# Performance work log

Measured on AMD Instinct MI355X. Metric: run time of the kernel, lower is better.

Reference implementation:

```python
import jax, jax.numpy as jnp
import numpy as np
import math

D_MODEL = 1024
EMB = 1024

def setup_inputs() -> dict:
    key = jax.random.key(0)
    ks = jax.random.split(key, 9)
    s = 1.0 / math.sqrt(EMB)
    x = jax.random.normal(ks[0], (4, 2048, EMB), dtype=jnp.float32)
    W1 = jax.random.uniform(ks[1], (EMB, EMB), minval=-s, maxval=s)
    b1 = jax.random.uniform(ks[2], (EMB,), minval=-s, maxval=s)
    W2 = jax.random.uniform(ks[3], (EMB, EMB), minval=-s, maxval=s)
    b2 = jax.random.uniform(ks[4], (EMB,), minval=-s, maxval=s)
    W3 = jax.random.uniform(ks[5], (EMB, EMB), minval=-s, maxval=s)
    b3 = jax.random.uniform(ks[6], (EMB,), minval=-s, maxval=s)
    W4 = jax.random.uniform(ks[7], (EMB, EMB), minval=-s, maxval=s)
    b4 = jax.random.uniform(ks[8], (EMB,), minval=-s, maxval=s)
    return {"x": x, "W1": W1, "b1": b1, "W2": W2, "b2": b2,
            "W3": W3, "b3": b3, "W4": W4, "b4": b4}

def reference(x, W1, b1, W2, b2, W3, b3, W4, b4):
    # Q, K, V projections (torch Linear: x @ W.T + b; here W stored as [in, out])
    Q = x @ W1 + b1          # [B, S, E]
    K = x @ W2 + b2
    V = x @ W3 + b3
    scale = 1.0 / math.sqrt(D_MODEL)
    scores = jnp.einsum('bse,bte->bst', Q, K) * scale   # [B, S, S]
    attn = jax.nn.softmax(scores, axis=-1)
    out = jnp.einsum('bst,bte->bse', attn, V)           # [B, S, E]
    return out @ W4 + b4
```

## Files before the change

kernel.cpp:

```cpp
#include <hip/hip_runtime.h>
#include <hip/hip_bf16.h>

typedef __attribute__((ext_vector_type(4))) float f32x4;
typedef __attribute__((ext_vector_type(8))) short bf16x8;

__device__ __forceinline__ void gload_lds16(const void* g, void* l) {
  __builtin_amdgcn_global_load_lds(
      (const __attribute__((address_space(1))) void*)g,
      (__attribute__((address_space(3))) void*)l, 16, 0, 0);
}

__device__ __forceinline__ unsigned short f2bf(float f) {
  union { float f; unsigned u; } x; x.f = f;
  unsigned r = x.u + 0x7fffu + ((x.u >> 16) & 1u);
  return (unsigned short)(r >> 16);
}

__device__ __forceinline__ float bf2f(unsigned short s) {
  union { unsigned u; float f; } x; x.u = (unsigned)s << 16;
  return x.f;
}

template<int N> __device__ __forceinline__ void vm_wait();
template<> __device__ __forceinline__ void vm_wait<0>() { asm volatile("s_waitcnt vmcnt(0)" ::: "memory"); }
template<> __device__ __forceinline__ void vm_wait<4>() { asm volatile("s_waitcnt vmcnt(4)" ::: "memory"); }
template<> __device__ __forceinline__ void vm_wait<6>() { asm volatile("s_waitcnt vmcnt(6)" ::: "memory"); }

#define BARRIER() asm volatile("s_barrier" ::: "memory")
#define SCHED0()  __builtin_amdgcn_sched_barrier(0)

template<int BN, int EPI, bool OUT_F32>
__global__ __launch_bounds__(512, 2)
void gemm256(const unsigned short* __restrict__ A,
             const unsigned short* __restrict__ Bt,
             const float* __restrict__ bias,
             float* __restrict__ rs,
             void* __restrict__ Cout,
             int K, int lda, int ldb, int ldc, float alpha,
             long sA, long sB, long sC)
{
  constexpr int THREADS = 512;
  constexpr int WN = BN / 64;
  constexpr int WM = 8 / WN;
  constexpr int WTM = 256 / WM;
  constexpr int M_REP = WTM / 16;
  constexpr int MH = M_REP / 2;
  constexpr int ABUFE = 256 * 64;
  constexpr int BBUFE = BN * 64;
  constexpr int BBASE = 2 * ABUFE;
  constexpr int LOADS_A = 2;
  constexpr int LOADS_B = BN / 128;
  constexpr int VM_STEADY = 2 * LOADS_B + LOADS_A;

  __shared__ __attribute__((aligned(16))) unsigned short lds[BBASE + 2 * BBUFE];

  const int gx = gridDim.x, gy = gridDim.y;
  const int lid = blockIdx.x + gx * (blockIdx.y + gy * blockIdx.z);
  const int nwg = gx * gy * gridDim.z;
  const int q = nwg >> 3, r = nwg & 7;
  const int xcd = lid & 7, idx = lid >> 3;
  const int nl = (xcd < r ? xcd * (q + 1) : r * (q + 1) + (xcd - r) * q) + idx;
  const int bx = nl % gx, by = (nl / gx) % gy, bz = nl / (gx * gy);

  const int tid = threadIdx.x, wave = tid >> 6, lane = tid & 63;
  const int wr = wave / WN, wc = wave % WN;
  const int fr = lane & 15, fq = lane >> 4, sw = fr & 7;

  A  += (size_t)bz * sA;
  Bt += (size_t)bz * sB;
  const int m0 = by * 256;
  const int n0 = bx * BN;
  const int NT = K >> 6;

  f32x4 acc[M_REP][4] = {};
  bf16x8 a[MH][2], b[4][2];

  auto stageA = [&](int t, int half) {
#pragma unroll
    for (int c = 0; c < LOADS_A; ++c) {
      const int s = c * THREADS + tid;
      const int rr = s >> 3;
      const int col = ((tid & 7) ^ (rr & 7)) * 8;
      gload_lds16(A + (size_t)(m0 + half * 128 + rr) * lda + t * 64 + col,
                  &lds[(t & 1) * ABUFE + half * (128 * 64) + s * 8]);
    }
  };
  auto stageB = [&](int t, int half) {
#pragma unroll
    for (int c = 0; c < LOADS_B; ++c) {
      const int s = c * THREADS + tid;
      const int rr = s >> 3;
      const int col = ((tid & 7) ^ (rr & 7)) * 8;
      gload_lds16(Bt + (size_t)(n0 + half * (BN / 2) + rr) * ldb + t * 64 + col,
                  &lds[BBASE + (t & 1) * BBUFE + half * ((BN / 2) * 64) + s * 8]);
    }
  };
  auto readA = [&](int buf, int mq) {
    const unsigned short* p = &lds[buf * ABUFE];
#pragma unroll
    for (int mm = 0; mm < MH; ++mm)
#pragma unroll
      for (int kk = 0; kk < 2; ++kk)
        a[mm][kk] = *(const bf16x8*)(p + (wr * WTM + mq * (WTM / 2) + mm * 16 + fr) * 64
                                       + ((kk * 4 + fq) ^ sw) * 8);
  };
  auto readB = [&](int buf, int nh) {
    const unsigned short* p = &lds[BBASE + buf * BBUFE];
#pragma unroll
    for (int nn = 0; nn < 2; ++nn)
#pragma unroll
      for (int kk = 0; kk < 2; ++kk)
        b[nh * 2 + nn][kk] = *(const bf16x8*)(p + (wc * 64 + (nh * 2 + nn) * 16 + fr) * 64
                                                + ((kk * 4 + fq) ^ sw) * 8);
  };
  auto mfmaQ = [&](int mq, int nh) {
    __builtin_amdgcn_s_setprio(1);
#pragma unroll
    for (int kk = 0; kk < 2; ++kk)
#pragma unroll
      for (int mm = 0; mm < MH; ++mm)
#pragma unroll
        for (int nn = 0; nn < 2; ++nn)
          acc[mq * MH + mm][nh * 2 + nn] = __builtin_amdgcn_mfma_f32_16x16x32_bf16(
              a[mm][kk], b[nh * 2 + nn][kk], acc[mq * MH + mm][nh * 2 + nn], 0, 0, 0);
    __builtin_amdgcn_s_setprio(0);
  };

  stageA(0, 0); stageA(0, 1); stageB(0, 0); stageB(0, 1);
  if (NT > 1) { stageB(1, 0); stageB(1, 1); stageA(1, 0); vm_wait<VM_STEADY>(); }
  else        { vm_wait<0>(); }
  BARRIER();

  for (int t = 0; t < NT; ++t) {
    const int buf = t & 1;
    readA(buf, 0); readB(buf, 0);
    BARRIER(); SCHED0();
    mfmaQ(0, 0);
    SCHED0();
    BARRIER();
    readB(buf, 1);
    if (t + 1 < NT) stageA(t + 1, 1);
    BARRIER(); SCHED0();
    mfmaQ(0, 1);
    SCHED0();
    BARRIER();
    readA(buf, 1);
    if (t + 2 < NT) stageB(t + 2, 0);
    BARRIER(); SCHED0();
    mfmaQ(1, 0);
    SCHED0();
    BARRIER();
    if (t + 2 < NT) { stageB(t + 2, 1); stageA(t + 2, 0); vm_wait<VM_STEADY>(); }
    else            { vm_wait<0>(); }
    BARRIER(); SCHED0();
    mfmaQ(1, 1);
    SCHED0();
    BARRIER();
  }

  float bvc[4];
  if (EPI == 5) {
#pragma unroll
    for (int nn = 0; nn < 4; ++nn) bvc[nn] = bias[n0 + wc * 64 + nn * 16 + fr];
  }
  if (EPI == 3) {
#pragma unroll
    for (int nn = 0; nn < 4; ++nn)
      bvc[nn] = bias[(size_t)bz * 2048 + n0 + wc * 64 + nn * 16 + fr];
  }
#pragma unroll
  for (int mm = 0; mm < M_REP; ++mm) {
    const int rbase = m0 + wr * WTM + mm * 16 + fq * 4;
#pragma unroll
    for (int j = 0; j < 4; ++j) {
      const int row = rbase + j;
      float rsc = 1.f;
      if (EPI == 5) rsc = __builtin_amdgcn_rcpf(rs[(size_t)bz * 2048 + row]);
      float part = 0.f;
#pragma unroll
      for (int nn = 0; nn < 4; ++nn) {
        const int col = n0 + wc * 64 + nn * 16 + fr;
        float v = acc[mm][nn][j];
        if      (EPI == 3) { v = __expf((v + bvc[nn]) * alpha); part += v; }
        else if (EPI == 5) v = v * rsc + bvc[nn];
        else               v = v * alpha;
        const size_t off = (size_t)bz * sC + (size_t)row * ldc + col;
        if (OUT_F32) ((float*)Cout)[off] = v;
        else         ((unsigned short*)Cout)[off] = f2bf(v);
      }
      if (EPI == 3) {
        part += __shfl_xor(part, 1); part += __shfl_xor(part, 2);
        part += __shfl_xor(part, 4); part += __shfl_xor(part, 8);
        if (fr == 0) atomicAdd(rs + (size_t)bz * 2048 + row, part);
      }
    }
  }
}

__global__ __launch_bounds__(256, 2)
void prep_gemm(const unsigned short* __restrict__ W2b, const unsigned short* __restrict__ W1b,
               const unsigned short* __restrict__ W4t, const unsigned short* __restrict__ W3b,
               unsigned short* __restrict__ Mtb, unsigned short* __restrict__ W34tb)
{
  __shared__ __attribute__((aligned(16))) unsigned short As[128 * 32];
  __shared__ __attribute__((aligned(16))) unsigned short Bs[128 * 32];
  const int which = blockIdx.z;
  const unsigned short* A  = which ? W4t : W2b;
  const unsigned short* Bt = which ? W3b : W1b;
  unsigned short* C = which ? W34tb : Mtb;

  const int tid = threadIdx.x, wave = tid >> 6, lane = tid & 63;
  const int m0 = blockIdx.y * 128, n0 = blockIdx.x * 128;
  f32x4 acc[4][4] = {};
  const int wr = wave >> 1, wc = wave & 1;
  const int fr = lane & 15, fq = lane >> 4;
  const int si0 = wave * 2, sr = lane >> 2, sce = (lane & 3) * 8;

  for (int k0 = 0; k0 < 1024; k0 += 32) {
#pragma unroll
    for (int c = 0; c < 2; ++c) {
      const int i = si0 + c, rr = i * 16 + sr;
      gload_lds16(A  + (size_t)(m0 + rr) * 1024 + k0 + sce, As + i * 512 + lane * 8);
      gload_lds16(Bt + (size_t)(n0 + rr) * 1024 + k0 + sce, Bs + i * 512 + lane * 8);
    }
    __syncthreads();
    bf16x8 af[4], bg[4];
#pragma unroll
    for (int m = 0; m < 4; ++m)
      af[m] = *(const bf16x8*)(As + (wr * 64 + m * 16 + fr) * 32 + fq * 8);
#pragma unroll
    for (int n = 0; n < 4; ++n)
      bg[n] = *(const bf16x8*)(Bs + (wc * 64 + n * 16 + fr) * 32 + fq * 8);
#pragma unroll
    for (int m = 0; m < 4; ++m)
#pragma unroll
      for (int n = 0; n < 4; ++n)
        acc[m][n] = __builtin_amdgcn_mfma_f32_16x16x32_bf16(af[m], bg[n], acc[m][n], 0, 0, 0);
    __syncthreads();
  }
#pragma unroll
  for (int m = 0; m < 4; ++m) {
    const int rbase = m0 + wr * 64 + m * 16 + fq * 4;
#pragma unroll
    for (int j = 0; j < 4; ++j)
#pragma unroll
      for (int n = 0; n < 4; ++n) {
        const int col = n0 + wc * 64 + n * 16 + fr;
        C[(size_t)(rbase + j) * 1024 + col] = f2bf(acc[m][n][j]);
      }
  }
}

__global__ __launch_bounds__(256)
void convert_kernel(const float* __restrict__ x, unsigned short* __restrict__ xb)
{
  const int idx = (blockIdx.x * 256 + threadIdx.x) * 8;
  const float4 a = *(const float4*)(x + idx);
  const float4 b = *(const float4*)(x + idx + 4);
  unsigned u0 = (unsigned)f2bf(a.x) | ((unsigned)f2bf(a.y) << 16);
  unsigned u1 = (unsigned)f2bf(a.z) | ((unsigned)f2bf(a.w) << 16);
  unsigned u2 = (unsigned)f2bf(b.x) | ((unsigned)f2bf(b.y) << 16);
  unsigned u3 = (unsigned)f2bf(b.z) | ((unsigned)f2bf(b.w) << 16);
  uint4 o; o.x = u0; o.y = u1; o.z = u2; o.w = u3;
  *(uint4*)(xb + idx) = o;
}

__global__ __launch_bounds__(256)
void convert3_kernel(const float* __restrict__ a, const float* __restrict__ b,
                     const float* __restrict__ c,
                     unsigned short* __restrict__ oa, unsigned short* __restrict__ ob,
                     unsigned short* __restrict__ oc)
{
  const float* src = (blockIdx.y == 0) ? a : (blockIdx.y == 1) ? b : c;
  unsigned short* dst = (blockIdx.y == 0) ? oa : (blockIdx.y == 1) ? ob : oc;
  const int idx = (blockIdx.x * 256 + threadIdx.x) * 8;
  const float4 p = *(const float4*)(src + idx);
  const float4 q = *(const float4*)(src + idx + 4);
  unsigned u0 = (unsigned)f2bf(p.x) | ((unsigned)f2bf(p.y) << 16);
  unsigned u1 = (unsigned)f2bf(p.z) | ((unsigned)f2bf(p.w) << 16);
  unsigned u2 = (unsigned)f2bf(q.x) | ((unsigned)f2bf(q.y) << 16);
  unsigned u3 = (unsigned)f2bf(q.z) | ((unsigned)f2bf(q.w) << 16);
  uint4 o; o.x = u0; o.y = u1; o.z = u2; o.w = u3;
  *(uint4*)(dst + idx) = o;
}

__global__ __launch_bounds__(256)
void transpose_w4_kernel(const float* __restrict__ W, unsigned short* __restrict__ out)
{
  __shared__ float t[64][65];
  const int k0 = blockIdx.y * 64;
  const int n0 = blockIdx.x * 64;
  const int tx = threadIdx.x & 63, ty = threadIdx.x >> 6;
#pragma unroll
  for (int r = ty; r < 64; r += 4)
    t[r][tx] = W[(size_t)(k0 + r) * 1024 + n0 + tx];
  __syncthreads();
#pragma unroll
  for (int r = ty; r < 64; r += 4)
    out[(size_t)(n0 + r) * 1024 + k0 + tx] = f2bf(t[tx][r]);
}

__global__ __launch_bounds__(256)
void prep_vec_kernel(const float* __restrict__ W2, const float* __restrict__ b1,
                     const unsigned short* __restrict__ W4t,
                     const float* __restrict__ b3, const float* __restrict__ b4,
                     float* __restrict__ w21, float* __restrict__ bfv)
{
  const int e = blockIdx.x * 4 + (threadIdx.x >> 6);
  const int lane = threadIdx.x & 63;
  float acc = 0.f;
  if (blockIdx.y == 0) {
#pragma unroll 4
    for (int i = 0; i < 16; ++i) {
      const int n = i * 64 + lane;
      acc += W2[(size_t)e * 1024 + n] * b1[n];
    }
#pragma unroll
    for (int o = 32; o; o >>= 1) acc += __shfl_xor(acc, o);
    if (lane == 0) w21[e] = acc;
  } else {
#pragma unroll 4
    for (int i = 0; i < 16; ++i) {
      const int j = i * 64 + lane;
      acc += bf2f(W4t[(size_t)e * 1024 + j]) * b3[j];
    }
#pragma unroll
    for (int o = 32; o; o >>= 1) acc += __shfl_xor(acc, o);
    if (lane == 0) bfv[e] = acc + b4[e];
  }
}

__global__ __launch_bounds__(256)
void v_kernel(const unsigned short* __restrict__ xb, const float* __restrict__ w21,
              float* __restrict__ v)
{
  const int i = blockIdx.x * 4 + (threadIdx.x >> 6);
  const int lane = threadIdx.x & 63;
  float acc = 0.f;
  const unsigned short* row = xb + (size_t)i * 1024;
#pragma unroll 2
  for (int it = 0; it < 2; ++it) {
    const int k0 = (it * 64 + lane) * 8;
    bf16x8 pk = *(const bf16x8*)(row + k0);
#pragma unroll
    for (int j = 0; j < 8; ++j)
      acc += bf2f(((const unsigned short*)&pk)[j]) * w21[k0 + j];
  }
#pragma unroll
  for (int o = 32; o; o >>= 1) acc += __shfl_xor(acc, o);
  if (lane == 0) v[i] = acc;
}

extern "C" void kernel_launch(void* const* d_in, const int* in_sizes, int n_in,
                              void* d_out, int out_size, void* d_ws, size_t ws_size,
                              hipStream_t stream)
{
  const float* x  = (const float*)d_in[0];
  const float* W1 = (const float*)d_in[1];
  const float* b1 = (const float*)d_in[2];
  const float* W2 = (const float*)d_in[3];
  const float* W3 = (const float*)d_in[5];
  const float* b3 = (const float*)d_in[6];
  const float* W4 = (const float*)d_in[7];
  const float* b4 = (const float*)d_in[8];

  char* ws = (char*)d_ws;
  const size_t MB = 1024 * 1024;
  unsigned short* xb    = (unsigned short*)(ws);
  unsigned short* W4t   = (unsigned short*)(ws + 16 * MB);
  unsigned short* W2b   = (unsigned short*)(ws + 18 * MB);
  unsigned short* W1b   = (unsigned short*)(ws + 20 * MB);
  unsigned short* W3b   = (unsigned short*)(ws + 22 * MB);
  unsigned short* G     = (unsigned short*)(ws + 24 * MB);
  unsigned short* Mtb   = (unsigned short*)(ws + 40 * MB);
  unsigned short* W34tb = (unsigned short*)(ws + 42 * MB);
  float*          rsum  = (float*)(ws + 44 * MB);
  float*          bfv   = (float*)(ws + 45 * MB);
  float*          w21   = (float*)(ws + 45 * MB + 8192);
  float*          vvec  = (float*)(ws + 45 * MB + 16384);
  unsigned short* Vt    = (unsigned short*)(ws + 56 * MB);
  unsigned short* S     = (unsigned short*)(ws + 72 * MB);

  convert_kernel<<<4096, 256, 0, stream>>>(x, xb);
  convert3_kernel<<<dim3(512, 3), 256, 0, stream>>>(W1, W2, W3, W1b, W2b, W3b);
  transpose_w4_kernel<<<dim3(16, 16), 256, 0, stream>>>(W4, W4t);

  prep_gemm<<<dim3(8, 8, 2), 256, 0, stream>>>(W2b, W1b, W4t, W3b, Mtb, W34tb);

  prep_vec_kernel<<<dim3(256, 2), 256, 0, stream>>>(W2, b1, W4t, b3, b4, w21, bfv);

  gemm256<128, 0, false><<<dim3(8, 32, 1), 512, 0, stream>>>(
      xb, Mtb, nullptr, nullptr, G, 1024, 1024, 1024, 1024, 1.f, 0, 0, 0);

  gemm256<128, 0, false><<<dim3(16, 4, 4), 512, 0, stream>>>(
      W34tb, xb, nullptr, nullptr, Vt, 1024, 1024, 1024, 2048, 1.f,
      0, 2048L * 1024, 1024L * 2048);

  v_kernel<<<2048, 256, 0, stream>>>(xb, w21, vvec);

  hipMemsetAsync(rsum, 0, 4 * 2048 * sizeof(float), stream);

  gemm256<256, 3, false><<<dim3(8, 8, 4), 512, 0, stream>>>(
      G, xb, vvec, rsum, S, 1024, 1024, 1024, 2048, 0.03125f,
      2048L * 1024, 2048L * 1024, 2048L * 2048);

  gemm256<128, 5, true><<<dim3(8, 8, 4), 512, 0, stream>>>(
      S, Vt, bfv, rsum, d_out, 2048, 2048, 2048, 1024, 1.f,
      2048L * 2048, 1024L * 2048, 2048L * 1024);
}
```

Before: 184.8 us.

## Merge small prep kernels and fuse the two projection GEMMs into one launch

Several small launches are combined into fewer kernels with blockIdx-based dispatch. The weight convert, W4 transpose and bias-vector kernels become one weights_prep kernel. The Mt/W34t prep GEMM, the v-vector kernel and the rsum memset become prep2, and the G and Vt projection GEMMs run as one 512-block dual launch. This cuts launch overhead and idle tails between dependent small kernels and lets the two projection GEMMs share the GPU at the same time. The bfv vector is now computed from fp32 W4 rather than the bf16 transposed copy, which changes rounding slightly. Heterogeneous blocks in one grid can cause load imbalance.

```diff
diff --git a/kernel.cpp b/kernel.cpp
--- a/kernel.cpp
+++ b/kernel.cpp
@@ -30,14 +30,15 @@
 #define SCHED0()  __builtin_amdgcn_sched_barrier(0)
 
 template<int BN, int EPI, bool OUT_F32>
-__global__ __launch_bounds__(512, 2)
-void gemm256(const unsigned short* __restrict__ A,
-             const unsigned short* __restrict__ Bt,
-             const float* __restrict__ bias,
-             float* __restrict__ rs,
-             void* __restrict__ Cout,
-             int K, int lda, int ldb, int ldc, float alpha,
-             long sA, long sB, long sC)
+__device__ __forceinline__ void gemm_body(
+    const unsigned short* __restrict__ A,
+    const unsigned short* __restrict__ Bt,
+    const float* __restrict__ bias,
+    float* __restrict__ rs,
+    void* __restrict__ Cout,
+    int K, int lda, int ldb, int ldc, float alpha,
+    long sA, long sB, long sC,
+    int bx, int by, int bz, unsigned short* lds)
 {
   constexpr int THREADS = 512;
   constexpr int WN = BN / 64;
@@ -51,16 +52,6 @@
   constexpr int LOADS_A = 2;
   constexpr int LOADS_B = BN / 128;
   constexpr int VM_STEADY = 2 * LOADS_B + LOADS_A;
-
-  __shared__ __attribute__((aligned(16))) unsigned short lds[BBASE + 2 * BBUFE];
-
-  const int gx = gridDim.x, gy = gridDim.y;
-  const int lid = blockIdx.x + gx * (blockIdx.y + gy * blockIdx.z);
-  const int nwg = gx * gy * gridDim.z;
-  const int q = nwg >> 3, r = nwg & 7;
-  const int xcd = lid & 7, idx = lid >> 3;
-  const int nl = (xcd < r ? xcd * (q + 1) : r * (q + 1) + (xcd - r) * q) + idx;
-  const int bx = nl % gx, by = (nl / gx) % gy, bz = nl / (gx * gy);
 
   const int tid = threadIdx.x, wave = tid >> 6, lane = tid & 63;
   const int wr = wave / WN, wc = wave % WN;
@@ -197,57 +188,50 @@
   }
 }
 
-__global__ __launch_bounds__(256, 2)
-void prep_gemm(const unsigned short* __restrict__ W2b, const unsigned short* __restrict__ W1b,
-               const unsigned short* __restrict__ W4t, const unsigned short* __restrict__ W3b,
-               unsigned short* __restrict__ Mtb, unsigned short* __restrict__ W34tb)
-{
-  __shared__ __attribute__((aligned(16))) unsigned short As[128 * 32];
-  __shared__ __attribute__((aligned(16))) unsigned short Bs[128 * 32];
-  const int which = blockIdx.z;
-  const unsigned short* A  = which ? W4t : W2b;
-  const unsigned short* Bt = which ? W3b : W1b;
-  unsigned short* C = which ? W34tb : Mtb;
-
-  const int tid = threadIdx.x, wave = tid >> 6, lane = tid & 63;
-  const int m0 = blockIdx.y * 128, n0 = blockIdx.x * 128;
-  f32x4 acc[4][4] = {};
-  const int wr = wave >> 1, wc = wave & 1;
-  const int fr = lane & 15, fq = lane >> 4;
-  const int si0 = wave * 2, sr = lane >> 2, sce = (lane & 3) * 8;
-
-  for (int k0 = 0; k0 < 1024; k0 += 32) {
-#pragma unroll
-    for (int c = 0; c < 2; ++c) {
-      const int i = si0 + c, rr = i * 16 + sr;
-      gload_lds16(A  + (size_t)(m0 + rr) * 1024 + k0 + sce, As + i * 512 + lane * 8);
-      gload_lds16(Bt + (size_t)(n0 + rr) * 1024 + k0 + sce, Bs + i * 512 + lane * 8);
-    }
-    __syncthreads();
-    bf16x8 af[4], bg[4];
-#pragma unroll
-    for (int m = 0; m < 4; ++m)
-      af[m] = *(const bf16x8*)(As + (wr * 64 + m * 16 + fr) * 32 + fq * 8);
-#pragma unroll
-    for (int n = 0; n < 4; ++n)
-      bg[n] = *(const bf16x8*)(Bs + (wc * 64 + n * 16 + fr) * 32 + fq * 8);
-#pragma unroll
-    for (int m = 0; m < 4; ++m)
-#pragma unroll
-      for (int n = 0; n < 4; ++n)
-        acc[m][n] = __builtin_amdgcn_mfma_f32_16x16x32_bf16(af[m], bg[n], acc[m][n], 0, 0, 0);
-    __syncthreads();
-  }
-#pragma unroll
-  for (int m = 0; m < 4; ++m) {
-    const int rbase = m0 + wr * 64 + m * 16 + fq * 4;
-#pragma unroll
-    for (int j = 0; j < 4; ++j)
-#pragma unroll
-      for (int n = 0; n < 4; ++n) {
-        const int col = n0 + wc * 64 + n * 16 + fr;
-        C[(size_t)(rbase + j) * 1024 + col] = f2bf(acc[m][n][j]);
-      }
+__device__ __forceinline__ int xcd_swz(int lid, int nwg) {
+  const int q = nwg >> 3, r = nwg & 7;
+  const int xcd = lid & 7, idx = lid >> 3;
+  return (xcd < r ? xcd * (q + 1) : r * (q + 1) + (xcd - r) * q) + idx;
+}
+
+template<int BN, int EPI, bool OUT_F32>
+__global__ __launch_bounds__(512, 2)
+void gemm256(const unsigned short* __restrict__ A,
+             const unsigned short* __restrict__ Bt,
+             const float* __restrict__ bias,
+             float* __restrict__ rs,
+             void* __restrict__ Cout,
+             int K, int lda, int ldb, int ldc, float alpha,
+             long sA, long sB, long sC)
+{
+  __shared__ __attribute__((aligned(16))) unsigned short lds[2 * 256 * 64 + 2 * BN * 64];
+  const int gx = gridDim.x, gy = gridDim.y;
+  const int lid = blockIdx.x + gx * (blockIdx.y + gy * blockIdx.z);
+  const int nl = xcd_swz(lid, gx * gy * gridDim.z);
+  const int bx = nl % gx, by = (nl / gx) % gy, bz = nl / (gx * gy);
+  gemm_body<BN, EPI, OUT_F32>(A, Bt, bias, rs, Cout, K, lda, ldb, ldc, alpha,
+                              sA, sB, sC, bx, by, bz, lds);
+}
+
+__global__ __launch_bounds__(512, 2)
+void gemm256_dual(const unsigned short* __restrict__ A0, const unsigned short* __restrict__ B0,
+                  void* __restrict__ C0,
+                  const unsigned short* __restrict__ A1, const unsigned short* __restrict__ B1,
+                  void* __restrict__ C1,
+                  long sA1, long sB1, long sC1)
+{
+  __shared__ __attribute__((aligned(16))) unsigned short lds[2 * 256 * 64 + 2 * 128 * 64];
+  const int f = blockIdx.x;
+  if (f < 256) {
+    const int nl = xcd_swz(f, 256);
+    const int bx = nl & 7, by = nl >> 3;
+    gemm_body<128, 0, false>(A0, B0, nullptr, nullptr, C0,
+                             1024, 1024, 1024, 1024, 1.f, 0, 0, 0, bx, by, 0, lds);
+  } else {
+    const int nl = xcd_swz(f - 256, 256);
+    const int bx = nl & 15, by = (nl >> 4) & 3, bz = nl >> 6;
+    gemm_body<128, 0, false>(A1, B1, nullptr, nullptr, C1,
+                             1024, 1024, 1024, 2048, 1.f, sA1, sB1, sC1, bx, by, bz, lds);
   }
 }
 
@@ -266,50 +250,54 @@
 }
 
 __global__ __launch_bounds__(256)
-void convert3_kernel(const float* __restrict__ a, const float* __restrict__ b,
-                     const float* __restrict__ c,
-                     unsigned short* __restrict__ oa, unsigned short* __restrict__ ob,
-                     unsigned short* __restrict__ oc)
-{
-  const float* src = (blockIdx.y == 0) ? a : (blockIdx.y == 1) ? b : c;
-  unsigned short* dst = (blockIdx.y == 0) ? oa : (blockIdx.y == 1) ? ob : oc;
-  const int idx = (blockIdx.x * 256 + threadIdx.x) * 8;
-  const float4 p = *(const float4*)(src + idx);
-  const float4 q = *(const float4*)(src + idx + 4);
-  unsigned u0 = (unsigned)f2bf(p.x) | ((unsigned)f2bf(p.y) << 16);
-  unsigned u1 = (unsigned)f2bf(p.z) | ((unsigned)f2bf(p.w) << 16);
-  unsigned u2 = (unsigned)f2bf(q.x) | ((unsigned)f2bf(q.y) << 16);
-  unsigned u3 = (unsigned)f2bf(q.z) | ((unsigned)f2bf(q.w) << 16);
-  uint4 o; o.x = u0; o.y = u1; o.z = u2; o.w = u3;
-  *(uint4*)(dst + idx) = o;
-}
-
-__global__ __launch_bounds__(256)
-void transpose_w4_kernel(const float* __restrict__ W, unsigned short* __restrict__ out)
+void weights_prep(const float* __restrict__ W1, const float* __restrict__ W2,
+                  const float* __restrict__ W3, const float* __restrict__ W4,
+                  const float* __restrict__ b1, const float* __restrict__ b3,
+                  const float* __restrict__ b4,
+                  unsigned short* __restrict__ W1b, unsigned short* __restrict__ W2b,
+                  unsigned short* __restrict__ W3b, unsigned short* __restrict__ W4t,
+                  float* __restrict__ w21, float* __restrict__ bfv)
 {
   __shared__ float t[64][65];
-  const int k0 = blockIdx.y * 64;
-  const int n0 = blockIdx.x * 64;
-  const int tx = threadIdx.x & 63, ty = threadIdx.x >> 6;
-#pragma unroll
-  for (int r = ty; r < 64; r += 4)
-    t[r][tx] = W[(size_t)(k0 + r) * 1024 + n0 + tx];
-  __syncthreads();
-#pragma unroll
-  for (int r = ty; r < 64; r += 4)
-    out[(size_t)(n0 + r) * 1024 + k0 + tx] = f2bf(t[tx][r]);
-}
-
-__global__ __launch_bounds__(256)
-void prep_vec_kernel(const float* __restrict__ W2, const float* __restrict__ b1,
-                     const unsigned short* __restrict__ W4t,
-                     const float* __restrict__ b3, const float* __restrict__ b4,
-                     float* __restrict__ w21, float* __restrict__ bfv)
-{
-  const int e = blockIdx.x * 4 + (threadIdx.x >> 6);
-  const int lane = threadIdx.x & 63;
-  float acc = 0.f;
-  if (blockIdx.y == 0) {
+  const int f = blockIdx.x, tid = threadIdx.x;
+  if (f < 1536) {
+    const int which = f >> 9, blk = f & 511;
+    const float* src = (which == 0) ? W1 : (which == 1) ? W2 : W3;
+    unsigned short* dst = (which == 0) ? W1b : (which == 1) ? W2b : W3b;
+    const int idx = (blk * 256 + tid) * 8;
+    const float4 p = *(const float4*)(src + idx);
+    const float4 q = *(const float4*)(src + idx + 4);
+    unsigned u0 = (unsigned)f2bf(p.x) | ((unsigned)f2bf(p.y) << 16);
+    unsigned u1 = (unsigned)f2bf(p.z) | ((unsigned)f2bf(p.w) << 16);
+    unsigned u2 = (unsigned)f2bf(q.x) | ((unsigned)f2bf(q.y) << 16);
+    unsigned u3 = (unsigned)f2bf(q.z) | ((unsigned)f2bf(q.w) << 16);
+    uint4 o; o.x = u0; o.y = u1; o.z = u2; o.w = u3;
+    *(uint4*)(dst + idx) = o;
+  } else if (f < 1792) {
+    const int tb = f - 1536;
+    const int k0 = (tb >> 4) * 64, n0 = (tb & 15) * 64;
+    const int tx = tid & 63, ty = tid >> 6;
+#pragma unroll
+    for (int r = ty; r < 64; r += 4)
+      t[r][tx] = W4[(size_t)(k0 + r) * 1024 + n0 + tx];
+    __syncthreads();
+#pragma unroll
+    for (int r = ty; r < 64; r += 4)
+      W4t[(size_t)(n0 + r) * 1024 + k0 + tx] = f2bf(t[tx][r]);
+  } else if (f < 1808) {
+    const int e0 = (f - 1792) * 64;
+    const int tx = tid & 63, ty = tid >> 6;
+    float acc = 0.f;
+    for (int j = ty; j < 1024; j += 4)
+      acc += b3[j] * W4[(size_t)j * 1024 + e0 + tx];
+    t[ty][tx] = acc;
+    __syncthreads();
+    if (ty == 0)
+      bfv[e0 + tx] = t[0][tx] + t[1][tx] + t[2][tx] + t[3][tx] + b4[e0 + tx];
+  } else {
+    const int e = (f - 1808) * 4 + (tid >> 6);
+    const int lane = tid & 63;
+    float acc = 0.f;
 #pragma unroll 4
     for (int i = 0; i < 16; ++i) {
       const int n = i * 64 + lane;
@@ -318,37 +306,87 @@
 #pragma unroll
     for (int o = 32; o; o >>= 1) acc += __shfl_xor(acc, o);
     if (lane == 0) w21[e] = acc;
+  }
+}
+
+__global__ __launch_bounds__(256, 2)
+void prep2(const unsigned short* __restrict__ W2b, const unsigned short* __restrict__ W1b,
+           const unsigned short* __restrict__ W4t, const unsigned short* __restrict__ W3b,
+           unsigned short* __restrict__ Mtb, unsigned short* __restrict__ W34tb,
+           const unsigned short* __restrict__ xb, const float* __restrict__ w21,
+           float* __restrict__ vvec, float* __restrict__ rsum)
+{
+  __shared__ __attribute__((aligned(16))) unsigned short As[128 * 32];
+  __shared__ __attribute__((aligned(16))) unsigned short Bs[128 * 32];
+  const int f = blockIdx.x, tid = threadIdx.x;
+  if (f < 128) {
+    const int which = f >> 6, blk = f & 63;
+    const unsigned short* A  = which ? W4t : W2b;
+    const unsigned short* Bt = which ? W3b : W1b;
+    unsigned short* C = which ? W34tb : Mtb;
+    const int m0 = (blk >> 3) * 128, n0 = (blk & 7) * 128;
+    const int wave = tid >> 6, lane = tid & 63;
+    f32x4 acc[4][4] = {};
+    const int wr = wave >> 1, wc = wave & 1;
+    const int fr = lane & 15, fq = lane >> 4;
+    const int si0 = wave * 2, sr = lane >> 2, sce = (lane & 3) * 8;
+    for (int k0 = 0; k0 < 1024; k0 += 32) {
+#pragma unroll
+      for (int c = 0; c < 2; ++c) {
+        const int i = si0 + c, rr = i * 16 + sr;
+        gload_lds16(A  + (size_t)(m0 + rr) * 1024 + k0 + sce, As + i * 512 + lane * 8);
+        gload_lds16(Bt + (size_t)(n0 + rr) * 1024 + k0 + sce, Bs + i * 512 + lane * 8);
+      }
+      __syncthreads();
+      bf16x8 af[4], bg[4];
+#pragma unroll
+      for (int m = 0; m < 4; ++m)
+        af[m] = *(const bf16x8*)(As + (wr * 64 + m * 16 + fr) * 32 + fq * 8);
+#pragma unroll
+      for (int n = 0; n < 4; ++n)
+        bg[n] = *(const bf16x8*)(Bs + (wc * 64 + n * 16 + fr) * 32 + fq * 8);
+#pragma unroll
+      for (int m = 0; m < 4; ++m)
+#pragma unroll
+        for (int n = 0; n < 4; ++n)
+          acc[m][n] = __builtin_amdgcn_mfma_f32_16x16x32_bf16(af[m], bg[n], acc[m][n], 0, 0, 0);
+      __syncthreads();
+    }
+#pragma unroll
+    for (int m = 0; m < 4; ++m) {
+      const int rbase = m0 + wr * 64 + m * 16 + fq * 4;
+#pragma unroll
+      for (int j = 0; j < 4; ++j)
+#pragma unroll
+        for (int n = 0; n < 4; ++n)
+          C[(size_t)(rbase + j) * 1024 + (n0 + wc * 64 + n * 16 + fr)] = f2bf(acc[m][n][j]);
+    }
   } else {
+    const int f2 = f - 128;
+    if (f2 < 4) {
+      uint4 z = {0, 0, 0, 0};
+      float* p = rsum + f2 * 2048 + tid * 8;
+      *(uint4*)p = z; *(uint4*)(p + 4) = z;
+    }
+    const int wave = tid >> 6, lane = tid & 63;
 #pragma unroll 4
-    for (int i = 0; i < 16; ++i) {
-      const int j = i * 64 + lane;
-      acc += bf2f(W4t[(size_t)e * 1024 + j]) * b3[j];
-    }
-#pragma unroll
-    for (int o = 32; o; o >>= 1) acc += __shfl_xor(acc, o);
-    if (lane == 0) bfv[e] = acc + b4[e];
-  }
-}
-
-__global__ __launch_bounds__(256)
-void v_kernel(const unsigned short* __restrict__ xb, const float* __restrict__ w21,
-              float* __restrict__ v)
-{
-  const int i = blockIdx.x * 4 + (threadIdx.x >> 6);
-  const int lane = threadIdx.x & 63;
-  float acc = 0.f;
-  const unsigned short* row = xb + (size_t)i * 1024;
+    for (int rr = 0; rr < 4; ++rr) {
+      const int i = f2 * 16 + wave * 4 + rr;
+      const unsigned short* row = xb + (size_t)i * 1024;
+      float acc = 0.f;
 #pragma unroll 2
-  for (int it = 0; it < 2; ++it) {
-    const int k0 = (it * 64 + lane) * 8;
-    bf16x8 pk = *(const bf16x8*)(row + k0);
-#pragma unroll
-    for (int j = 0; j < 8; ++j)
-      acc += bf2f(((const unsigned short*)&pk)[j]) * w21[k0 + j];
-  }
-#pragma unroll
-  for (int o = 32; o; o >>= 1) acc += __shfl_xor(acc, o);
-  if (lane == 0) v[i] = acc;
+      for (int it = 0; it < 2; ++it) {
+        const int k0 = (it * 64 + lane) * 8;
+        bf16x8 pk = *(const bf16x8*)(row + k0);
+#pragma unroll
+        for (int j = 0; j < 8; ++j)
+          acc += bf2f(((const unsigned short*)&pk)[j]) * w21[k0 + j];
+      }
+#pragma unroll
+      for (int o = 32; o; o >>= 1) acc += __shfl_xor(acc, o);
+      if (lane == 0) vvec[i] = acc;
+    }
+  }
 }
 
 extern "C" void kernel_launch(void* const* d_in, const int* in_sizes, int n_in,
@@ -382,23 +420,14 @@
   unsigned short* S     = (unsigned short*)(ws + 72 * MB);
 
   convert_kernel<<<4096, 256, 0, stream>>>(x, xb);
-  convert3_kernel<<<dim3(512, 3), 256, 0, stream>>>(W1, W2, W3, W1b, W2b, W3b);
-  transpose_w4_kernel<<<dim3(16, 16), 256, 0, stream>>>(W4, W4t);
-
-  prep_gemm<<<dim3(8, 8, 2), 256, 0, stream>>>(W2b, W1b, W4t, W3b, Mtb, W34tb);
-
-  prep_vec_kernel<<<dim3(256, 2), 256, 0, stream>>>(W2, b1, W4t, b3, b4, w21, bfv);
-
-  gemm256<128, 0, false><<<dim3(8, 32, 1), 512, 0, stream>>>(
-      xb, Mtb, nullptr, nullptr, G, 1024, 1024, 1024, 1024, 1.f, 0, 0, 0);
-
-  gemm256<128, 0, false><<<dim3(16, 4, 4), 512, 0, stream>>>(
-      W34tb, xb, nullptr, nullptr, Vt, 1024, 1024, 1024, 2048, 1.f,
-      0, 2048L * 1024, 1024L * 2048);
-
-  v_kernel<<<2048, 256, 0, stream>>>(xb, w21, vvec);
-
-  hipMemsetAsync(rsum, 0, 4 * 2048 * sizeof(float), stream);
+
+  weights_prep<<<2064, 256, 0, stream>>>(W1, W2, W3, W4, b1, b3, b4,
+                                         W1b, W2b, W3b, W4t, w21, bfv);
+
+  prep2<<<640, 256, 0, stream>>>(W2b, W1b, W4t, W3b, Mtb, W34tb, xb, w21, vvec, rsum);
+
+  gemm256_dual<<<512, 512, 0, stream>>>(xb, Mtb, G, W34tb, xb, Vt,
+                                        0, 2048L * 1024, 1024L * 2048);
 
   gemm256<256, 3, false><<<dim3(8, 8, 4), 512, 0, stream>>>(
       G, xb, vvec, rsum, S, 1024, 1024, 1024, 2048, 0.03125f,
```

Measured after the change: 196.1 us. 6.1% more time.
